# Kernel tuning notes

Measured on AMD Instinct MI355X. Metric: run time of the kernel, lower is better.

The kernel has to match this reference:

```python
import jax, jax.numpy as jnp
import numpy as np

N_NODES = 20000
N_EDGES = 160000
N_GRAPHS = 1000
IN_DIM = 11
HID = 128
EDGE_DIM = 3
N_LAYERS = 5
BN_EPS = 1e-5


def setup_inputs() -> dict:
    key = jax.random.key(0)
    ks = jax.random.split(key, 24)
    x = jax.random.normal(ks[0], (N_NODES, IN_DIM), dtype=jnp.float32)
    edge_index = jax.random.randint(ks[1], (2, N_EDGES), 0, N_NODES, dtype=jnp.int64)
    batch = jnp.sort(jax.random.randint(ks[2], (N_NODES,), 0, N_GRAPHS, dtype=jnp.int64))
    edge_attr = jax.random.uniform(ks[3], (N_EDGES, EDGE_DIM), dtype=jnp.float32)
    s_in = 1.0 / np.sqrt(IN_DIM)
    s_z = 1.0 / np.sqrt(2 * HID + EDGE_DIM)
    s_h = 1.0 / np.sqrt(HID)
    W_in = jax.random.uniform(ks[4], (IN_DIM, HID), minval=-s_in, maxval=s_in)
    b_in = jax.random.uniform(ks[5], (HID,), minval=-s_in, maxval=s_in)
    Wf = jax.random.uniform(ks[6], (N_LAYERS, 2 * HID + EDGE_DIM, HID), minval=-s_z, maxval=s_z)
    bf = jax.random.uniform(ks[7], (N_LAYERS, HID), minval=-s_z, maxval=s_z)
    Ws = jax.random.uniform(ks[8], (N_LAYERS, 2 * HID + EDGE_DIM, HID), minval=-s_z, maxval=s_z)
    bs = jax.random.uniform(ks[9], (N_LAYERS, HID), minval=-s_z, maxval=s_z)
    gamma = jnp.ones((N_LAYERS, HID), dtype=jnp.float32)
    beta = jnp.zeros((N_LAYERS, HID), dtype=jnp.float32)
    W1 = jax.random.uniform(ks[10], (HID, HID), minval=-s_h, maxval=s_h)
    b1 = jax.random.uniform(ks[11], (HID,), minval=-s_h, maxval=s_h)
    W2 = jax.random.uniform(ks[12], (HID, HID), minval=-s_h, maxval=s_h)
    b2 = jax.random.uniform(ks[13], (HID,), minval=-s_h, maxval=s_h)
    W3 = jax.random.uniform(ks[14], (HID, 1), minval=-s_h, maxval=s_h)
    b3 = jax.random.uniform(ks[15], (1,), minval=-s_h, maxval=s_h)
    return {"x": x, "edge_index": edge_index, "batch": batch, "edge_attr": edge_attr,
            "W_in": W_in, "b_in": b_in, "Wf": Wf, "bf": bf, "Ws": Ws, "bs": bs,
            "gamma": gamma, "beta": beta, "W1": W1, "b1": b1, "W2": W2, "b2": b2,
            "W3": W3, "b3": b3}


def reference(x, edge_index, batch, edge_attr, W_in, b_in, Wf, bf, Ws, bs,
              gamma, beta, W1, b1, W2, b2, W3, b3):
    src = edge_index[0]  # x_j (source / neighbor)
    dst = edge_index[1]  # x_i (target / aggregation index)
    # in-degree per node for mean aggregation (zero-degree -> divide by 1, yields 0)
    deg = jax.ops.segment_sum(jnp.ones((N_EDGES,), jnp.float32), dst, num_segments=N_NODES)
    deg = jnp.maximum(deg, 1.0)[:, None]

    h = x @ W_in + b_in  # [N, H]
    for l in range(N_LAYERS):
        # CGConv: z = [x_i, x_j, e]; msg = sigmoid(z Wf) * softplus(z Ws); residual + mean-aggr
        z = jnp.concatenate([h[dst], h[src], edge_attr], axis=-1)  # [E, 2H+D]
        msg = jax.nn.sigmoid(z @ Wf[l] + bf[l]) * jax.nn.softplus(z @ Ws[l] + bs[l])
        agg = jax.ops.segment_sum(msg, dst, num_segments=N_NODES) / deg
        h = h + agg
        # BatchNorm1d (training-mode batch stats, biased variance)
        mu = jnp.mean(h, axis=0)
        var = jnp.mean((h - mu) ** 2, axis=0)
        h = (h - mu) * jax.lax.rsqrt(var + BN_EPS) * gamma[l] + beta[l]
        h = jax.nn.relu(h)
        # dropout omitted (eval mode)

    # global mean pool over graphs
    cnt = jax.ops.segment_sum(jnp.ones((N_NODES,), jnp.float32), batch, num_segments=N_GRAPHS)
    g = jax.ops.segment_sum(h, batch, num_segments=N_GRAPHS) / jnp.maximum(cnt, 1.0)[:, None]

    g = jax.nn.relu(g @ W1 + b1)
    g = jax.nn.relu(g @ W2 + b2)
    return g @ W3 + b3  # [G, 1]
```

## Files before the change

kernel.cpp:

```cpp
#include <hip/hip_runtime.h>
#include <math.h>

#define NN 20000
#define NE 160000
#define NG 1000
#define IND 11
#define H 128
#define ED 3
#define NL 5
#define ZDH (259*128)
#define BN_EPSF 1e-5f
#define EPW 32
#define QR 16
#define GP 4
#define MBLK 313

#define DEG_BLKS ((NE + 255) / 256)
#define WPREP_BLKS ((NL * 512 * H + 255) / 256)
#define GB_BLKS ((NN + 255) / 256)
#define HIN_BLKS 512
#define PREP_GRID (DEG_BLKS + WPREP_BLKS + GB_BLKS + HIN_BLKS)

typedef unsigned short ushort_t;
typedef unsigned int uint_t;
typedef __attribute__((ext_vector_type(8))) short bf8_t;
typedef __attribute__((ext_vector_type(4))) float f4_t;

__device__ inline ushort_t f2bf(float x) {
    unsigned int u = __float_as_uint(x);
    unsigned int r = (u + 0x7fffu + ((u >> 16) & 1u)) >> 16;
    return (ushort_t)r;
}
__device__ inline float bf2f(ushort_t b) {
    return __uint_as_float(((unsigned int)b) << 16);
}

__global__ __launch_bounds__(256) void prep_fused(const int* __restrict__ dst,
                                                  int* __restrict__ degi,
                                                  const float* __restrict__ Wf,
                                                  const float* __restrict__ Ws,
                                                  ushort_t* __restrict__ Wt,
                                                  const float* __restrict__ x,
                                                  const float* __restrict__ Win,
                                                  const float* __restrict__ bin,
                                                  float* __restrict__ h,
                                                  const int* __restrict__ batch,
                                                  int* __restrict__ gstart) {
    int b = blockIdx.x;
    int tid = threadIdx.x;
    if (b < DEG_BLKS) {
        int e = b * 256 + tid;
        if (e < NE) atomicAdd(&degi[dst[e]], 1);
    } else if (b < DEG_BLKS + WPREP_BLKS) {
        int idx = (b - DEG_BLKS) * 256 + tid;
        if (idx < NL * 512 * H) {
            int k = idx & 127;
            int n = (idx >> 7) & 511;
            int l = idx >> 16;
            int t = n >> 7, j = n & 127;
            const float* W = (t == 0 || t == 2) ? Wf : Ws;
            int krow = (t < 2) ? k : (H + k);
            ushort_t val = f2bf(W[(size_t)l * ZDH + krow * H + j]);
            int nt = j >> 4, sub = j & 15;
            int ks = k >> 5, quad = (k >> 3) & 3, e2 = k & 7;
            int lane = quad * 16 + sub;
            Wt[(size_t)l * 65536 + (size_t)t * 16384 +
               (((nt * 4 + ks) * 64 + lane) * 8 + e2)] = val;
        }
    } else if (b < DEG_BLKS + WPREP_BLKS + GB_BLKS) {
        int n = (b - DEG_BLKS - WPREP_BLKS) * 256 + tid;
        if (n < NN) {
            int b0 = batch[n];
            int bn = (n + 1 < NN) ? batch[n + 1] : NG;
            if (n == 0)
                for (int t = 0; t <= b0; ++t) gstart[t] = 0;
            for (int t = b0 + 1; t <= bn; ++t) gstart[t] = n + 1;
        }
    } else {
        __shared__ float lw[IND * H];
        for (int i = tid; i < IND * H; i += 256) lw[i] = Win[i];
        __syncthreads();
        int j = tid & 127;
        float bj = bin[j];
        int rb = b - (DEG_BLKS + WPREP_BLKS + GB_BLKS);
        for (int n = rb * 2 + (tid >> 7); n < NN; n += HIN_BLKS * 2) {
            const float* xr = x + (size_t)n * IND;
            float acc = bj;
#pragma unroll
            for (int k = 0; k < IND; ++k) acc = fmaf(xr[k], lw[k * H + j], acc);
            h[(size_t)n * H + j] = acc;
        }
    }
}

__global__ __launch_bounds__(256) void reserve_kernel(const int* __restrict__ degi,
                                                      int* __restrict__ cursor,
                                                      float* __restrict__ invdeg,
                                                      int* __restrict__ counter) {
    int n = blockIdx.x * blockDim.x + threadIdx.x;
    int lane = threadIdx.x & 63;
    int v = (n < NN) ? degi[n] : 0;
    int x = v;
#pragma unroll
    for (int st = 1; st < 64; st <<= 1) {
        int y = __shfl_up(x, st, 64);
        if (lane >= st) x += y;
    }
    int total = __shfl(x, 63, 64);
    int base = 0;
    if (lane == 63) base = atomicAdd(counter, total);
    base = __shfl(base, 63, 64);
    if (n < NN) {
        cursor[n] = base + x - v;
        invdeg[n] = 1.0f / (float)(v < 1 ? 1 : v);
    }
}

__global__ void scatter_kernel(const int* __restrict__ src, const int* __restrict__ dst,
                               const float* __restrict__ ea,
                               const float* __restrict__ invdeg,
                               int* __restrict__ cursor, float4* __restrict__ csr_ea4,
                               int* __restrict__ csr_dst, float* __restrict__ csr_inv) {
    int e = blockIdx.x * blockDim.x + threadIdx.x;
    if (e < NE) {
        int d = dst[e];
        int pos = atomicAdd(&cursor[d], 1);
        float4 r;
        r.x = ea[e * ED + 0];
        r.y = ea[e * ED + 1];
        r.z = ea[e * ED + 2];
        r.w = __int_as_float(src[e]);
        csr_ea4[pos] = r;
        csr_dst[pos] = d;
        csr_inv[pos] = invdeg[d];
    }
}

__global__ void flag_kernel(const int* __restrict__ csr_dst, unsigned* __restrict__ endmask) {
    int e = blockIdx.x * blockDim.x + threadIdx.x;
    if (e < NE) {
        int d = csr_dst[e];
        int dn = (e + 1 < NE) ? csr_dst[e + 1] : -1;
        if (d != dn) atomicOr(&endmask[e >> 5], 1u << (e & 31));
    }
}

__global__ __launch_bounds__(256, 4) void node_gemm_mfma(const float* __restrict__ hsrc,
                                                         float* __restrict__ hbn,
                                                         const ushort_t* __restrict__ Wt_l,
                                                         const float* __restrict__ sum,
                                                         const float* __restrict__ sumsq,
                                                         const float* __restrict__ gamma_l,
                                                         const float* __restrict__ beta_l,
                                                         int applyBN,
                                                         uint_t* __restrict__ ppack,
                                                         uint_t* __restrict__ qpack) {
    int pair = blockIdx.y;
    int tid = threadIdx.x;
    int wave = tid >> 6;
    int lane = tid & 63;
    int sub = lane & 15;
    int quad = lane >> 4;
    int m0 = blockIdx.x * 64 + wave * 16;
    int writeH = applyBN && (pair == 0);

    __shared__ float bnsc[H];
    __shared__ float bnsh[H];
    if (applyBN) {
        if (tid < H) {
            float mu  = sum[tid] * (1.0f / NN);
            float var = sumsq[tid] * (1.0f / NN) - mu * mu;
            float sc  = gamma_l[tid] * rsqrtf(var + BN_EPSF);
            bnsc[tid] = sc;
            bnsh[tid] = beta_l[tid] - mu * sc;
        }
        __syncthreads();
    }

    const bf8_t* fragF = (const bf8_t*)(Wt_l + (size_t)(2 * pair) * 16384);
    const bf8_t* fragS = (const bf8_t*)(Wt_l + (size_t)(2 * pair + 1) * 16384);

    bf8_t aHi[4], aLo[4];
    int r = m0 + sub;
    int rc = r < NN ? r : NN - 1;
#pragma unroll
    for (int ks = 0; ks < 4; ++ks) {
        int kb = ks * 32 + quad * 8;
        const float* hp = hsrc + (size_t)rc * H + kb;
        float4 v0 = *(const float4*)hp;
        float4 v1 = *(const float4*)(hp + 4);
        float vv[8] = {v0.x, v0.y, v0.z, v0.w, v1.x, v1.y, v1.z, v1.w};
        if (applyBN) {
#pragma unroll
            for (int i = 0; i < 8; ++i) {
                float v = fmaf(vv[i], bnsc[kb + i], bnsh[kb + i]);
                vv[i] = v > 0.0f ? v : 0.0f;
            }
        }
        bf8_t hi8, lo8;
#pragma unroll
        for (int i = 0; i < 8; ++i) {
            ushort_t hi = f2bf(vv[i]);
            hi8[i] = (short)hi;
            lo8[i] = (short)f2bf(vv[i] - bf2f(hi));
        }
        aHi[ks] = hi8;
        aLo[ks] = lo8;
        if (writeH && r < NN) {
            float* op = hbn + (size_t)r * H + kb;
            *(float4*)op = make_float4(vv[0], vv[1], vv[2], vv[3]);
            *(float4*)(op + 4) = make_float4(vv[4], vv[5], vv[6], vv[7]);
        }
    }

    f4_t accF[8], accS[8];
#pragma unroll
    for (int b = 0; b < 8; ++b) { accF[b] = (f4_t){0.f, 0.f, 0.f, 0.f}; accS[b] = (f4_t){0.f, 0.f, 0.f, 0.f}; }

#pragma unroll
    for (int nt = 0; nt < 8; ++nt) {
#pragma unroll
        for (int ks = 0; ks < 4; ++ks) {
            bf8_t bF = fragF[(nt * 4 + ks) * 64 + lane];
            bf8_t bS = fragS[(nt * 4 + ks) * 64 + lane];
            accF[nt] = __builtin_amdgcn_mfma_f32_16x16x32_bf16(aHi[ks], bF, accF[nt], 0, 0, 0);
            accF[nt] = __builtin_amdgcn_mfma_f32_16x16x32_bf16(aLo[ks], bF, accF[nt], 0, 0, 0);
            accS[nt] = __builtin_amdgcn_mfma_f32_16x16x32_bf16(aHi[ks], bS, accS[nt], 0, 0, 0);
            accS[nt] = __builtin_amdgcn_mfma_f32_16x16x32_bf16(aLo[ks], bS, accS[nt], 0, 0, 0);
        }
    }

    uint_t* outp = pair ? qpack : ppack;
#pragma unroll
    for (int nt = 0; nt < 8; ++nt) {
        int col = nt * 16 + sub;
#pragma unroll
        for (int rr = 0; rr < 4; ++rr) {
            int row = m0 + quad * 4 + rr;
            if (row < NN) {
                uint_t lo = f2bf(accF[nt][rr]);
                uint_t hi = f2bf(accS[nt][rr]);
                outp[(size_t)row * H + col] = lo | (hi << 16);
            }
        }
    }
}

__global__ __launch_bounds__(256) void agg_edge_kernel(const int4* __restrict__ csr_fe,
                                                       const int* __restrict__ csr_dst,
                                                       const float* __restrict__ csr_inv,
                                                       const unsigned* __restrict__ endmask,
                                                       const float* __restrict__ Wf,
                                                       const float* __restrict__ bf,
                                                       const float* __restrict__ Ws,
                                                       const float* __restrict__ bs,
                                                       const uint_t* __restrict__ ppack,
                                                       const uint_t* __restrict__ qpack,
                                                       float* __restrict__ h,
                                                       float* __restrict__ sum,
                                                       float* __restrict__ sumsq) {
    int tid = threadIdx.x;
    if (blockIdx.x == 0 && tid < H) { sum[tid] = 0.0f; sumsq[tid] = 0.0f; }
    int lane = tid & 63;
    int wv = tid >> 6;
    int base = (blockIdx.x * 4 + wv) * EPW;
    int c0 = 2 * lane;

    float2 wf0 = *(const float2*)&Wf[256 * H + c0];
    float2 wf1 = *(const float2*)&Wf[257 * H + c0];
    float2 wf2 = *(const float2*)&Wf[258 * H + c0];
    float2 ws0 = *(const float2*)&Ws[256 * H + c0];
    float2 ws1 = *(const float2*)&Ws[257 * H + c0];
    float2 ws2 = *(const float2*)&Ws[258 * H + c0];
    float2 bf2_ = *(const float2*)&bf[c0];
    float2 bs2_ = *(const float2*)&bs[c0];

    int4 fe = csr_fe[base + (lane & (EPW - 1))];
    int  dd = csr_dst[base + (lane & (EPW - 1))];
    int  ivr = __float_as_int(csr_inv[base + (lane & (EPW - 1))]);
    unsigned mask = __builtin_amdgcn_readfirstlane(endmask[base >> 5]);

    uint2 q[QR];
#pragma unroll
    for (int i = 0; i < QR; ++i) {
        int s = __builtin_amdgcn_readlane(fe.w, i);
        q[i] = *(const uint2*)&qpack[(size_t)s * H + c0];
    }

    int dcur = __builtin_amdgcn_readlane(dd, 0);
    uint2 ppc = *(const uint2*)&ppack[(size_t)dcur * H + c0];
    float pf0 = __uint_as_float(ppc.x << 16), ps0 = __uint_as_float(ppc.x & 0xFFFF0000u);
    float pf1 = __uint_as_float(ppc.y << 16), ps1 = __uint_as_float(ppc.y & 0xFFFF0000u);
    unsigned m = mask;
    int e0 = m ? __builtin_ctz(m) : EPW;
    int dnext = 0;
    uint2 ppN = ppc;
    if (e0 + 1 < EPW) {
        dnext = __builtin_amdgcn_readlane(dd, e0 + 1);
        ppN = *(const uint2*)&ppack[(size_t)dnext * H + c0];
    }

    float acc0 = 0.f, acc1 = 0.f;

#pragma unroll
    for (int tb = 0; tb < EPW; tb += 8) {
#pragma unroll
        for (int i = 0; i < 8; ++i) {
            int t = tb + i;
            float ex = __int_as_float(__builtin_amdgcn_readlane(fe.x, t));
            float ey = __int_as_float(__builtin_amdgcn_readlane(fe.y, t));
            float ez = __int_as_float(__builtin_amdgcn_readlane(fe.z, t));
            uint2 qq = q[t & (QR - 1)];
            if (t + QR < EPW) {
                int s2 = __builtin_amdgcn_readlane(fe.w, t + QR);
                q[t & (QR - 1)] = *(const uint2*)&qpack[(size_t)s2 * H + c0];
            }
            float qf0 = __uint_as_float(qq.x << 16);
            float qs0 = __uint_as_float(qq.x & 0xFFFF0000u);
            float qf1 = __uint_as_float(qq.y << 16);
            float qs1 = __uint_as_float(qq.y & 0xFFFF0000u);
            float f0 = fmaf(ex, wf0.x, fmaf(ey, wf1.x, fmaf(ez, wf2.x, pf0 + bf2_.x + qf0)));
            float v0 = fmaf(ex, ws0.x, fmaf(ey, ws1.x, fmaf(ez, ws2.x, ps0 + bs2_.x + qs0)));
            float f1 = fmaf(ex, wf0.y, fmaf(ey, wf1.y, fmaf(ez, wf2.y, pf1 + bf2_.y + qf1)));
            float v1 = fmaf(ex, ws0.y, fmaf(ey, ws1.y, fmaf(ez, ws2.y, ps1 + bs2_.y + qs1)));
            float sig0 = __builtin_amdgcn_rcpf(1.0f + __expf(-f0));
            float sp0  = fmaxf(v0, 0.0f) + __logf(1.0f + __expf(-fabsf(v0)));
            float sig1 = __builtin_amdgcn_rcpf(1.0f + __expf(-f1));
            float sp1  = fmaxf(v1, 0.0f) + __logf(1.0f + __expf(-fabsf(v1)));
            acc0 = fmaf(sig0, sp0, acc0);
            acc1 = fmaf(sig1, sp1, acc1);
            if (mask & (1u << t)) {
                float inv = __int_as_float(__builtin_amdgcn_readlane(ivr, t));
                atomicAdd(&h[(size_t)dcur * H + c0], acc0 * inv);
                atomicAdd(&h[(size_t)dcur * H + c0 + 1], acc1 * inv);
                acc0 = 0.f; acc1 = 0.f;
                dcur = dnext;
                pf0 = __uint_as_float(ppN.x << 16); ps0 = __uint_as_float(ppN.x & 0xFFFF0000u);
                pf1 = __uint_as_float(ppN.y << 16); ps1 = __uint_as_float(ppN.y & 0xFFFF0000u);
                m &= m - 1;
                int e1 = m ? __builtin_ctz(m) : EPW;
                if (e1 + 1 < EPW) {
                    dnext = __builtin_amdgcn_readlane(dd, e1 + 1);
                    ppN = *(const uint2*)&ppack[(size_t)dnext * H + c0];
                }
            }
        }
    }
    if (!(mask & (1u << (EPW - 1)))) {
        float inv = __int_as_float(__builtin_amdgcn_readlane(ivr, EPW - 1));
        atomicAdd(&h[(size_t)dcur * H + c0], acc0 * inv);
        atomicAdd(&h[(size_t)dcur * H + c0 + 1], acc1 * inv);
    }
}

__global__ __launch_bounds__(H) void stats_kernel(const float* __restrict__ h,
                                                  float* __restrict__ sum,
                                                  float* __restrict__ sumsq) {
    int j = threadIdx.x;
    float s = 0.0f, ss = 0.0f;
    int n = blockIdx.x * 8;
    for (; n + 7 < NN; n += gridDim.x * 8) {
        float v[8];
#pragma unroll
        for (int i = 0; i < 8; ++i) v[i] = h[(size_t)(n + i) * H + j];
#pragma unroll
        for (int i = 0; i < 8; ++i) { s += v[i]; ss = fmaf(v[i], v[i], ss); }
    }
    for (; n < NN; ++n) {
        float v = h[(size_t)n * H + j];
        s += v;
        ss = fmaf(v, v, ss);
    }
    atomicAdd(&sum[j], s);
    atomicAdd(&sumsq[j], ss);
}

__global__ __launch_bounds__(H) void pool_mlp_kernel(const float* __restrict__ h,
                                                     const int* __restrict__ gstart,
                                                     const float* __restrict__ sum,
                                                     const float* __restrict__ sumsq,
                                                     const float* __restrict__ gamma,
                                                     const float* __restrict__ beta,
                                                     const float* __restrict__ W1,
                                                     const float* __restrict__ b1,
                                                     const float* __restrict__ W2,
                                                     const float* __restrict__ b2,
                                                     const float* __restrict__ W3,
                                                     const float* __restrict__ b3,
                                                     float* __restrict__ out) {
    int j = threadIdx.x;
    float mu  = sum[j] * (1.0f / NN);
    float var = sumsq[j] * (1.0f / NN) - mu * mu;
    float sc  = gamma[j] * rsqrtf(var + BN_EPSF);
    float sh  = beta[j] - mu * sc;

    __shared__ float s1[GP][H];
    __shared__ float s2[GP][H];

#pragma unroll
    for (int gi = 0; gi < GP; ++gi) {
        int g0 = blockIdx.x * GP + gi;
        int a = gstart[g0], e = gstart[g0 + 1];
        float p0 = 0.f, p1 = 0.f, p2 = 0.f, p3 = 0.f;
        int n = a;
        for (; n + 3 < e; n += 4) {
            float v0 = fmaf(h[(size_t)(n + 0) * H + j], sc, sh);
            float v1 = fmaf(h[(size_t)(n + 1) * H + j], sc, sh);
            float v2 = fmaf(h[(size_t)(n + 2) * H + j], sc, sh);
            float v3 = fmaf(h[(size_t)(n + 3) * H + j], sc, sh);
            p0 += fmaxf(v0, 0.f); p1 += fmaxf(v1, 0.f);
            p2 += fmaxf(v2, 0.f); p3 += fmaxf(v3, 0.f);
        }
        for (; n < e; ++n) {
            float v = fmaf(h[(size_t)n * H + j], sc, sh);
            p0 += fmaxf(v, 0.f);
        }
        float cf = (float)(e - a);
        if (cf < 1.f) cf = 1.f;
        s1[gi][j] = ((p0 + p1) + (p2 + p3)) / cf;
    }
    __syncthreads();

    float a1[GP];
#pragma unroll
    for (int gi = 0; gi < GP; ++gi) a1[gi] = b1[j];
    for (int k = 0; k < H; ++k) {
        float w = W1[k * H + j];
#pragma unroll
        for (int gi = 0; gi < GP; ++gi) a1[gi] = fmaf(s1[gi][k], w, a1[gi]);
    }
#pragma unroll
    for (int gi = 0; gi < GP; ++gi) s2[gi][j] = fmaxf(a1[gi], 0.f);
    __syncthreads();

#pragma unroll
    for (int gi = 0; gi < GP; ++gi) a1[gi] = b2[j];
    for (int k = 0; k < H; ++k) {
        float w = W2[k * H + j];
#pragma unroll
        for (int gi = 0; gi < GP; ++gi) a1[gi] = fmaf(s2[gi][k], w, a1[gi]);
    }

    float w3 = W3[j];
    __shared__ float wred[2][GP];
#pragma unroll
    for (int gi = 0; gi < GP; ++gi) {
        float p = fmaxf(a1[gi], 0.f) * w3;
        for (int off2 = 32; off2 > 0; off2 >>= 1) p += __shfl_down(p, off2, 64);
        if ((j & 63) == 0) wred[j >> 6][gi] = p;
    }
    __syncthreads();
    if (j < GP) out[blockIdx.x * GP + j] = wred[0][j] + wred[1][j] + b3[0];
}

extern "C" void kernel_launch(void* const* d_in, const int* in_sizes, int n_in,
                              void* d_out, int out_size, void* d_ws, size_t ws_size,
                              hipStream_t stream) {
    const float* x     = (const float*)d_in[0];
    const int*   ei    = (const int*)d_in[1];
    const int*   srcp  = ei;
    const int*   dstp  = ei + NE;
    const int*   batch = (const int*)d_in[2];
    const float* ea    = (const float*)d_in[3];
    const float* Win   = (const float*)d_in[4];
    const float* bin   = (const float*)d_in[5];
    const float* Wf    = (const float*)d_in[6];
    const float* bf    = (const float*)d_in[7];
    const float* Ws    = (const float*)d_in[8];
    const float* bs    = (const float*)d_in[9];
    const float* gamma = (const float*)d_in[10];
    const float* beta  = (const float*)d_in[11];
    const float* W1    = (const float*)d_in[12];
    const float* b1    = (const float*)d_in[13];
    const float* W2    = (const float*)d_in[14];
    const float* b2    = (const float*)d_in[15];
    const float* W3    = (const float*)d_in[16];
    const float* b3    = (const float*)d_in[17];
    float* out = (float*)d_out;

    const size_t NH = (size_t)NN * H;
    float* wsp = (float*)d_ws;
    size_t off = 0;
    float* hA     = wsp + off; off += NH;
    float* hB     = wsp + off; off += NH;
    uint_t* ppack = (uint_t*)(wsp + off); off += NH;
    uint_t* qpack = (uint_t*)(wsp + off); off += NH;
    float* invdeg = wsp + off; off += NN;
    float* sum    = wsp + off; off += H;
    float* sumsq  = wsp + off; off += H;
    int* gstart   = (int*)(wsp + off); off += NG + 1;
    off = (off + 3) & ~(size_t)3;
    float4* csr_ea4 = (float4*)(wsp + off); off += (size_t)NE * 4;
    float* csr_inv = wsp + off; off += NE;
    int* degi      = (int*)(wsp + off); off += NN;
    int* counter   = (int*)(wsp + off); off += 1;
    unsigned* endmask = (unsigned*)(wsp + off); off += NE / 32;
    int* cursor    = (int*)(wsp + off); off += NN;
    int* csr_dst   = (int*)(wsp + off); off += NE;
    off = (off + 3) & ~(size_t)3;
    ushort_t* Wt = (ushort_t*)(wsp + off); off += (size_t)NL * 512 * H / 2;

    hipMemsetAsync(degi, 0, (NN + 1 + NE / 32) * sizeof(int), stream);
    prep_fused<<<PREP_GRID, 256, 0, stream>>>(dstp, degi, Wf, Ws, Wt,
                                              x, Win, bin, hA, batch, gstart);
    reserve_kernel<<<(NN + 255) / 256, 256, 0, stream>>>(degi, cursor, invdeg, counter);
    scatter_kernel<<<(NE + 255) / 256, 256, 0, stream>>>(srcp, dstp, ea, invdeg, cursor,
                                                         csr_ea4, csr_dst, csr_inv);
    flag_kernel<<<(NE + 255) / 256, 256, 0, stream>>>(csr_dst, endmask);

    float* hRead = hA;
    for (int l = 0; l < NL; ++l) {
        float* hTgt = (l == 0) ? hA : ((l & 1) ? hB : hA);
        node_gemm_mfma<<<dim3(MBLK, 2), 256, 0, stream>>>(
            hRead, hTgt,
            Wt + (size_t)l * 512 * H,
            sum, sumsq,
            gamma + (size_t)(l ? l - 1 : 0) * H,
            beta  + (size_t)(l ? l - 1 : 0) * H,
            l > 0, ppack, qpack);
        agg_edge_kernel<<<NE / (4 * EPW), 256, 0, stream>>>((const int4*)csr_ea4, csr_dst,
                                                            csr_inv, endmask,
                                                            Wf + (size_t)l * ZDH, bf + (size_t)l * H,
                                                            Ws + (size_t)l * ZDH, bs + (size_t)l * H,
                                                            ppack, qpack,
                                                            hTgt, sum, sumsq);
        stats_kernel<<<512, H, 0, stream>>>(hTgt, sum, sumsq);
        hRead = hTgt;
    }

    pool_mlp_kernel<<<NG / GP, H, 0, stream>>>(hRead, gstart, sum, sumsq,
                                               gamma + (size_t)(NL - 1) * H,
                                               beta + (size_t)(NL - 1) * H,
                                               W1, b1, W2, b2, W3, b3, out);
}
```

Baseline: 461.1 us.

## Fold segment-end flags into reserve kernel and prefetch all source rows upfront

Measured after the change: 461.5 us. Within noise of the previous version (+0.1%).

```diff
diff --git a/kernel.cpp b/kernel.cpp
--- a/kernel.cpp
+++ b/kernel.cpp
@@ -11,7 +11,6 @@
 #define ZDH (259*128)
 #define BN_EPSF 1e-5f
 #define EPW 32
-#define QR 16
 #define GP 4
 #define MBLK 313
 
@@ -96,7 +95,8 @@
 __global__ __launch_bounds__(256) void reserve_kernel(const int* __restrict__ degi,
                                                       int* __restrict__ cursor,
                                                       float* __restrict__ invdeg,
-                                                      int* __restrict__ counter) {
+                                                      int* __restrict__ counter,
+                                                      unsigned* __restrict__ endmask) {
     int n = blockIdx.x * blockDim.x + threadIdx.x;
     int lane = threadIdx.x & 63;
     int v = (n < NN) ? degi[n] : 0;
@@ -111,8 +111,13 @@
     if (lane == 63) base = atomicAdd(counter, total);
     base = __shfl(base, 63, 64);
     if (n < NN) {
-        cursor[n] = base + x - v;
+        int st0 = base + x - v;
+        cursor[n] = st0;
         invdeg[n] = 1.0f / (float)(v < 1 ? 1 : v);
+        if (v > 0) {
+            int endp = st0 + v - 1;
+            atomicOr(&endmask[endp >> 5], 1u << (endp & 31));
+        }
     }
 }
 
@@ -133,15 +138,6 @@
         csr_ea4[pos] = r;
         csr_dst[pos] = d;
         csr_inv[pos] = invdeg[d];
-    }
-}
-
-__global__ void flag_kernel(const int* __restrict__ csr_dst, unsigned* __restrict__ endmask) {
-    int e = blockIdx.x * blockDim.x + threadIdx.x;
-    if (e < NE) {
-        int d = csr_dst[e];
-        int dn = (e + 1 < NE) ? csr_dst[e + 1] : -1;
-        if (d != dn) atomicOr(&endmask[e >> 5], 1u << (e & 31));
     }
 }
 
@@ -280,17 +276,19 @@
     int  ivr = __float_as_int(csr_inv[base + (lane & (EPW - 1))]);
     unsigned mask = __builtin_amdgcn_readfirstlane(endmask[base >> 5]);
 
-    uint2 q[QR];
-#pragma unroll
-    for (int i = 0; i < QR; ++i) {
+    uint2 q[EPW];
+#pragma unroll
+    for (int i = 0; i < EPW; ++i) {
         int s = __builtin_amdgcn_readlane(fe.w, i);
         q[i] = *(const uint2*)&qpack[(size_t)s * H + c0];
     }
 
     int dcur = __builtin_amdgcn_readlane(dd, 0);
     uint2 ppc = *(const uint2*)&ppack[(size_t)dcur * H + c0];
-    float pf0 = __uint_as_float(ppc.x << 16), ps0 = __uint_as_float(ppc.x & 0xFFFF0000u);
-    float pf1 = __uint_as_float(ppc.y << 16), ps1 = __uint_as_float(ppc.y & 0xFFFF0000u);
+    float pf0 = __uint_as_float(ppc.x << 16) + bf2_.x;
+    float ps0 = __uint_as_float(ppc.x & 0xFFFF0000u) + bs2_.x;
+    float pf1 = __uint_as_float(ppc.y << 16) + bf2_.y;
+    float ps1 = __uint_as_float(ppc.y & 0xFFFF0000u) + bs2_.y;
     unsigned m = mask;
     int e0 = m ? __builtin_ctz(m) : EPW;
     int dnext = 0;
@@ -310,19 +308,15 @@
             float ex = __int_as_float(__builtin_amdgcn_readlane(fe.x, t));
             float ey = __int_as_float(__builtin_amdgcn_readlane(fe.y, t));
             float ez = __int_as_float(__builtin_amdgcn_readlane(fe.z, t));
-            uint2 qq = q[t & (QR - 1)];
-            if (t + QR < EPW) {
-                int s2 = __builtin_amdgcn_readlane(fe.w, t + QR);
-                q[t & (QR - 1)] = *(const uint2*)&qpack[(size_t)s2 * H + c0];
-            }
+            uint2 qq = q[t];
             float qf0 = __uint_as_float(qq.x << 16);
             float qs0 = __uint_as_float(qq.x & 0xFFFF0000u);
             float qf1 = __uint_as_float(qq.y << 16);
             float qs1 = __uint_as_float(qq.y & 0xFFFF0000u);
-            float f0 = fmaf(ex, wf0.x, fmaf(ey, wf1.x, fmaf(ez, wf2.x, pf0 + bf2_.x + qf0)));
-            float v0 = fmaf(ex, ws0.x, fmaf(ey, ws1.x, fmaf(ez, ws2.x, ps0 + bs2_.x + qs0)));
-            float f1 = fmaf(ex, wf0.y, fmaf(ey, wf1.y, fmaf(ez, wf2.y, pf1 + bf2_.y + qf1)));
-            float v1 = fmaf(ex, ws0.y, fmaf(ey, ws1.y, fmaf(ez, ws2.y, ps1 + bs2_.y + qs1)));
+            float f0 = fmaf(ex, wf0.x, fmaf(ey, wf1.x, fmaf(ez, wf2.x, pf0 + qf0)));
+            float v0 = fmaf(ex, ws0.x, fmaf(ey, ws1.x, fmaf(ez, ws2.x, ps0 + qs0)));
+            float f1 = fmaf(ex, wf0.y, fmaf(ey, wf1.y, fmaf(ez, wf2.y, pf1 + qf1)));
+            float v1 = fmaf(ex, ws0.y, fmaf(ey, ws1.y, fmaf(ez, ws2.y, ps1 + qs1)));
             float sig0 = __builtin_amdgcn_rcpf(1.0f + __expf(-f0));
             float sp0  = fmaxf(v0, 0.0f) + __logf(1.0f + __expf(-fabsf(v0)));
             float sig1 = __builtin_amdgcn_rcpf(1.0f + __expf(-f1));
@@ -335,8 +329,10 @@
                 atomicAdd(&h[(size_t)dcur * H + c0 + 1], acc1 * inv);
                 acc0 = 0.f; acc1 = 0.f;
                 dcur = dnext;
-                pf0 = __uint_as_float(ppN.x << 16); ps0 = __uint_as_float(ppN.x & 0xFFFF0000u);
-                pf1 = __uint_as_float(ppN.y << 16); ps1 = __uint_as_float(ppN.y & 0xFFFF0000u);
+                pf0 = __uint_as_float(ppN.x << 16) + bf2_.x;
+                ps0 = __uint_as_float(ppN.x & 0xFFFF0000u) + bs2_.x;
+                pf1 = __uint_as_float(ppN.y << 16) + bf2_.y;
+                ps1 = __uint_as_float(ppN.y & 0xFFFF0000u) + bs2_.y;
                 m &= m - 1;
                 int e1 = m ? __builtin_ctz(m) : EPW;
                 if (e1 + 1 < EPW) {
@@ -503,10 +499,10 @@
     hipMemsetAsync(degi, 0, (NN + 1 + NE / 32) * sizeof(int), stream);
     prep_fused<<<PREP_GRID, 256, 0, stream>>>(dstp, degi, Wf, Ws, Wt,
                                               x, Win, bin, hA, batch, gstart);
-    reserve_kernel<<<(NN + 255) / 256, 256, 0, stream>>>(degi, cursor, invdeg, counter);
+    reserve_kernel<<<(NN + 255) / 256, 256, 0, stream>>>(degi, cursor, invdeg, counter,
+                                                         endmask);
     scatter_kernel<<<(NE + 255) / 256, 256, 0, stream>>>(srcp, dstp, ea, invdeg, cursor,
                                                          csr_ea4, csr_dst, csr_inv);
-    flag_kernel<<<(NE + 255) / 256, 256, 0, stream>>>(csr_dst, endmask);
 
     float* hRead = hA;
     for (int l = 0; l < NL; ++l) {
```
